# Kernel tuning notes

Hardware: AMD Instinct MI355X
Metric: run time of the kernel (lower is better)

## Reference

```python
import jax, jax.numpy as jnp
import numpy as np
from jax.scipy.linalg import expm

B, S, D_H, D_C = 8, 1024, 64, 3

def setup_inputs() -> dict:
    key = jax.random.key(0)
    k1, k2, k3 = jax.random.split(key, 3)
    x = jax.random.normal(k1, (B, S, D_H), dtype=jnp.float32)
    r_grid = jax.random.uniform(k2, (B, S, D_C), dtype=jnp.float32)
    L_param = jax.random.normal(k3, (D_C, D_H, D_H), dtype=jnp.float32)
    P_sp = jnp.eye(D_H, dtype=jnp.float32)  # allow_mixing=False -> identity buffer
    return {"x": x, "r_grid": r_grid, "L_param": L_param, "P_sp": P_sp}

def reference(x, r_grid, L_param, P_sp):
    # skew-symmetrize each generator: L_k <- 0.5*(L_k - L_k^T)
    L_skew = 0.5 * (L_param - jnp.swapaxes(L_param, -1, -2))      # [d_c, d_h, d_h]
    # A_r[b,s] = sum_k r_grid[b,s,k] * L_skew[k]
    A_r = jnp.einsum('bsk,kij->bsij', r_grid, L_skew)             # [B, S, d_h, d_h]
    # batched matrix exponential over leading dims
    R_r = expm(A_r)                                               # [B, S, d_h, d_h]
    R_eff = R_r @ P_sp                                            # [B, S, d_h, d_h]
    x_out = jnp.einsum('bsij,bsj->bsi', R_eff, x)                 # [B, S, d_h]
    return x_out
```

## Files before the change

### kernel.cpp

```cpp
#include <hip/hip_runtime.h>


typedef _Float16 half8 __attribute__((ext_vector_type(8)));
typedef __fp16 fp16x2 __attribute__((ext_vector_type(2)));
typedef float float4t __attribute__((ext_vector_type(4)));

union H2U { fp16x2 h; unsigned u; };

__device__ __forceinline__ unsigned pkrtz2(float a, float b) {
    H2U v; v.h = __builtin_amdgcn_cvt_pkrtz(a, b); return v.u;
}
__device__ __forceinline__ float h2lo(unsigned u) { H2U v; v.u = u; return (float)v.h[0]; }
__device__ __forceinline__ float h2hi(unsigned u) { H2U v; v.u = u; return (float)v.h[1]; }

__global__ void liepe_prep(const float* __restrict__ L, _Float16* __restrict__ wsA)
{
    int t = blockIdx.x * 256 + threadIdx.x;
    if (t >= 1536) return;
    int l   = t & 63;
    int f   = t >> 6;
    int kt  = f & 1;
    int m   = (f >> 1) & 3;
    int gen = f >> 3;
    int i   = 16 * m + (l & 15);
    int kk0 = 32 * kt + 8 * (l >> 4);
    const float* Lg = L + gen * 4096;
    half8 hi, lo;
    #pragma unroll
    for (int j = 0; j < 8; ++j) {
        int kk = kk0 + j;
        float d = Lg[i * 64 + kk] - Lg[kk * 64 + i];
        _Float16 h = (_Float16)d;
        hi[j] = h;
        lo[j] = (_Float16)(d - (float)h);
    }
    *(half8*)(wsA + f * 512 + l * 8) = hi;
    *(half8*)(wsA + 12288 + f * 512 + l * 8) = lo;
}


#define PSTR 36

#define STAGE_AND_LOAD_B()                                                       \
  {                                                                              \
    unsigned h0 = pkrtz2(b1[0], b1[1]);                                          \
    unsigned h1 = pkrtz2(b1[2], b1[3]);                                          \
    unsigned l0 = pkrtz2(b1[0] - h2lo(h0), b1[1] - h2hi(h0));                    \
    unsigned l1 = pkrtz2(b1[2] - h2lo(h1), b1[3] - h2hi(h1));                    \
    const int di = 8 * w + 2 * g;                                                \
    *(uint2*)&stage[buf][0][c][di] = make_uint2(h0, h1);                         \
    *(uint2*)&stage[buf][1][c][di] = make_uint2(l0, l1);                         \
    __syncthreads();                                                             \
    _Pragma("unroll")                                                            \
    for (int kt = 0; kt < 2; ++kt) {                                             \
      Bh[kt] = *(const half8*)&stage[buf][0][c][16 * kt + 4 * g];                \
      Bl[kt] = *(const half8*)&stage[buf][1][c][16 * kt + 4 * g];                \
    }                                                                            \
    buf ^= 1;                                                                    \
  }

#define GEMM_COMBINE(TOUT)                                                       \
  {                                                                              \
    _Pragma("unroll")                                                            \
    for (int gen = 0; gen < 3; ++gen) {                                          \
      float q = (gen == 0) ? q0 : ((gen == 1) ? q1 : q2);                        \
      float4t ac0 = {0.f, 0.f, 0.f, 0.f};                                        \
      float4t ac1 = {0.f, 0.f, 0.f, 0.f};                                        \
      ac0 = __builtin_amdgcn_mfma_f32_16x16x32_f16(Ah[gen*2+0], Bh[0], ac0, 0, 0, 0); \
      ac1 = __builtin_amdgcn_mfma_f32_16x16x32_f16(Ah[gen*2+1], Bh[1], ac1, 0, 0, 0); \
      ac0 = __builtin_amdgcn_mfma_f32_16x16x32_f16(Ah[gen*2+0], Bl[0], ac0, 0, 0, 0); \
      ac1 = __builtin_amdgcn_mfma_f32_16x16x32_f16(Ah[gen*2+1], Bl[1], ac1, 0, 0, 0); \
      ac0 = __builtin_amdgcn_mfma_f32_16x16x32_f16(Al[gen*2+0], Bh[0], ac0, 0, 0, 0); \
      ac1 = __builtin_amdgcn_mfma_f32_16x16x32_f16(Al[gen*2+1], Bh[1], ac1, 0, 0, 0); \
      _Pragma("unroll")                                                          \
      for (int r4 = 0; r4 < 4; ++r4) {                                           \
        float sum = ac0[r4] + ac1[r4];                                           \
        if (gen == 0) TOUT[r4] = q * sum;                                        \
        else          TOUT[r4] = fmaf(q, sum, TOUT[r4]);                         \
      }                                                                          \
    }                                                                            \
  }

__global__ __launch_bounds__(256) void liepe_mfma(
    const float* __restrict__ x,
    const float* __restrict__ r_grid,
    const _Float16* __restrict__ wsA,
    float* __restrict__ out,
    int n_tokens)
{
    __shared__ __align__(16) unsigned stage[2][2][16][PSTR];

    const int lane = threadIdx.x & 63;
    const int w    = threadIdx.x >> 6;
    const int c    = lane & 15;
    const int g    = lane >> 4;

    int tok = blockIdx.x * 16 + c;
    if (tok >= n_tokens) tok = n_tokens - 1;

    half8 Ah[6], Al[6];
    #pragma unroll
    for (int gen = 0; gen < 3; ++gen) {
        #pragma unroll
        for (int kt = 0; kt < 2; ++kt) {
            const int f = (gen * 4 + w) * 2 + kt;
            Ah[gen * 2 + kt] = *(const half8*)(wsA + f * 512 + lane * 8);
            Al[gen * 2 + kt] = *(const half8*)(wsA + 12288 + f * 512 + lane * 8);
        }
    }

    float xv[4];
    {
        float4 v = *(const float4*)(x + tok * 64 + 16 * w + 4 * g);
        xv[0] = v.x; xv[1] = v.y; xv[2] = v.z; xv[3] = v.w;
    }

    const float r0 = r_grid[tok * 3 + 0];
    const float r1 = r_grid[tok * 3 + 1];
    const float r2 = r_grid[tok * 3 + 2];
    const float sig2 = 0.5f * (r0 * r0 + r1 * r1 + r2 * r2);
    const float rho  = fmaf(17.3f, __builtin_sqrtf(sig2), 2.0f);
    const float inv_rho = 1.0f / rho;
    const int   M  = (int)rho + 14;
    const int   ms = M + 10;
    const float q0 = r0 * inv_rho, q1 = r1 * inv_rho, q2 = r2 * inv_rho;

    int maxM = M;
    #pragma unroll
    for (int off = 1; off < 64; off <<= 1)
        maxM = max(maxM, __shfl_xor(maxM, off));

    float jp = 0.f, jc = 0.f, N = 0.f;
    float b1[4] = {0.f, 0.f, 0.f, 0.f};
    float b2[4] = {0.f, 0.f, 0.f, 0.f};

    #pragma unroll 1
    for (int m = maxM + 10; m > maxM; --m) {
        bool sd = (m == ms);
        jc = sd ? 1e-12f : jc;
        jp = sd ? 0.f : jp;
        N  = sd ? (((m & 1) == 0) ? 2e-12f : 0.f) : N;
        float s = (jc > 1.0f) ? __builtin_amdgcn_rcpf(jc) : 1.0f;
        jc *= s; jp *= s; N *= s;
        float jm = fmaf((2.f * (float)m) * inv_rho, jc, -jp);
        jp = jc; jc = jm;
        int mm = m - 1;
        if ((mm & 1) == 0) N += (mm > 0) ? (jm + jm) : jm;
    }

    half8 Bh[2], Bl[2];
    int buf = 0;

    #pragma unroll 1
    for (int m = maxM; m >= 1; --m) {
        bool sd = (m == ms);
        jc = sd ? 1e-12f : jc;
        jp = sd ? 0.f : jp;
        N  = sd ? (((m & 1) == 0) ? 2e-12f : 0.f) : N;

        if (__any(jc > 2.0f)) {
            float s = (jc > 1.0f) ? __builtin_amdgcn_rcpf(jc) : 1.0f;
            jc *= s; jp *= s; N *= s;
            #pragma unroll
            for (int i = 0; i < 4; ++i) { b1[i] *= s; b2[i] *= s; }
        }

        STAGE_AND_LOAD_B();

        float t[4];
        GEMM_COMBINE(t);

        float cf = (m <= M) ? (jc + jc) : 0.f;
        #pragma unroll
        for (int i = 0; i < 4; ++i) {
            float bn = fmaf(cf, xv[i], t[i] + b2[i]);
            b2[i] = b1[i];
            b1[i] = bn;
        }

        float jm = fmaf((2.f * (float)m) * inv_rho, jc, -jp);
        jp = jc; jc = jm;
        int mm = m - 1;
        if ((mm & 1) == 0) N += (mm > 0) ? (jm + jm) : jm;
    }

    {
        STAGE_AND_LOAD_B();
        float t[4];
        GEMM_COMBINE(t);
        float4 v;
        float y0 = fmaf(jc, xv[0], t[0] + b2[0]);
        float y1 = fmaf(jc, xv[1], t[1] + b2[1]);
        float y2 = fmaf(jc, xv[2], t[2] + b2[2]);
        float y3 = fmaf(jc, xv[3], t[3] + b2[3]);
        v.x = (y0 - 0.5f * t[0]) / N;
        v.y = (y1 - 0.5f * t[1]) / N;
        v.z = (y2 - 0.5f * t[2]) / N;
        v.w = (y3 - 0.5f * t[3]) / N;
        *(float4*)(out + tok * 64 + 16 * w + 4 * g) = v;
    }
}

extern "C" void kernel_launch(void* const* d_in, const int* in_sizes, int n_in,
                              void* d_out, int out_size, void* d_ws, size_t ws_size,
                              hipStream_t stream) {
    const float* x = (const float*)d_in[0];
    const float* r = (const float*)d_in[1];
    const float* L = (const float*)d_in[2];
    float* out = (float*)d_out;
    _Float16* wsA = (_Float16*)d_ws;

    int n_tokens = in_sizes[0] / 64;

    liepe_prep<<<6, 256, 0, stream>>>(L, wsA);

    int nwg = (n_tokens + 15) / 16;
    liepe_mfma<<<nwg, 256, 0, stream>>>(x, r, wsA, out, n_tokens);
}
```

Baseline: 33.58 us.

## Unroll Clenshaw recurrence by two using precomputed generator products

The Bessel/Clenshaw recurrence now advances two steps per iteration. A new prep kernel precomputes the pairwise products of the skew generators (G_a G_b + G_b G_a), so each two-step update needs one barrier and a dependency chain of depth one instead of two serial matrix-vector stages. This halves the number of __syncthreads and sequential LDS round trips, but each iteration issues more MFMAs (12 matrix blocks versus 6), each thread holds 18 A-fragment pairs in registers, and occupancy is capped with waves_per_eu. The warp-uniform conditional rescale is replaced with an unconditional per-lane rescale.

```diff
diff --git a/kernel.cpp b/kernel.cpp
--- a/kernel.cpp
+++ b/kernel.cpp
@@ -13,82 +13,110 @@
 __device__ __forceinline__ float h2lo(unsigned u) { H2U v; v.u = u; return (float)v.h[0]; }
 __device__ __forceinline__ float h2hi(unsigned u) { H2U v; v.u = u; return (float)v.h[1]; }
 
-__global__ void liepe_prep(const float* __restrict__ L, _Float16* __restrict__ wsA)
+#define FRAG_LO 36864
+
+__global__ void liepe_prep_skew(const float* __restrict__ L, float* __restrict__ skew)
 {
     int t = blockIdx.x * 256 + threadIdx.x;
-    if (t >= 1536) return;
-    int l   = t & 63;
-    int f   = t >> 6;
-    int kt  = f & 1;
-    int m   = (f >> 1) & 3;
-    int gen = f >> 3;
-    int i   = 16 * m + (l & 15);
-    int kk0 = 32 * kt + 8 * (l >> 4);
-    const float* Lg = L + gen * 4096;
-    half8 hi, lo;
+    if (t >= 12288) return;
+    int k = t >> 12, rem = t & 4095, i = rem >> 6, j = rem & 63;
+    skew[t] = L[k * 4096 + i * 64 + j] - L[k * 4096 + j * 64 + i];
+}
+
+__global__ void liepe_prep_frags(const float* __restrict__ skew, _Float16* __restrict__ frag)
+{
+    const int p  = blockIdx.x >> 2;
+    const int m2 = blockIdx.x & 3;
+    __shared__ float Ga[4096], Gb[4096];
+    int a = 0, b = 0;
+    if (p >= 3) {
+        const int pa[6] = {0, 1, 2, 0, 0, 1};
+        const int pb[6] = {0, 1, 2, 1, 2, 2};
+        a = pa[p - 3]; b = pb[p - 3];
+        for (int idx = threadIdx.x; idx < 4096; idx += 256) {
+            Ga[idx] = skew[a * 4096 + idx];
+            Gb[idx] = skew[b * 4096 + idx];
+        }
+        __syncthreads();
+    }
     #pragma unroll
-    for (int j = 0; j < 8; ++j) {
-        int kk = kk0 + j;
-        float d = Lg[i * 64 + kk] - Lg[kk * 64 + i];
-        _Float16 h = (_Float16)d;
-        hi[j] = h;
-        lo[j] = (_Float16)(d - (float)h);
-    }
-    *(half8*)(wsA + f * 512 + l * 8) = hi;
-    *(half8*)(wsA + 12288 + f * 512 + l * 8) = lo;
+    for (int e4 = 0; e4 < 4; ++e4) {
+        int e = threadIdx.x * 4 + e4;
+        int kt = e >> 9, rem = e & 511, l = rem >> 3, j = rem & 7;
+        int i  = 16 * m2 + (l & 15);
+        int kk = 32 * kt + 8 * (l >> 4) + j;
+        float val;
+        if (p < 3) {
+            val = skew[p * 4096 + i * 64 + kk];
+        } else if (a == b) {
+            float acc = 0.f;
+            for (int t2 = 0; t2 < 64; ++t2)
+                acc += Ga[i * 64 + t2] * Ga[t2 * 64 + kk];
+            val = acc;
+        } else {
+            float acc = 0.f;
+            for (int t2 = 0; t2 < 64; ++t2)
+                acc += Ga[i * 64 + t2] * Gb[t2 * 64 + kk]
+                     + Gb[i * 64 + t2] * Ga[t2 * 64 + kk];
+            val = acc;
+        }
+        _Float16 h = (_Float16)val;
+        int f = p * 8 + m2 * 2 + kt;
+        frag[f * 512 + l * 8 + j] = h;
+        frag[FRAG_LO + f * 512 + l * 8 + j] = (_Float16)(val - (float)h);
+    }
 }
 
 
 #define PSTR 36
 
-#define STAGE_AND_LOAD_B()                                                       \
-  {                                                                              \
-    unsigned h0 = pkrtz2(b1[0], b1[1]);                                          \
-    unsigned h1 = pkrtz2(b1[2], b1[3]);                                          \
-    unsigned l0 = pkrtz2(b1[0] - h2lo(h0), b1[1] - h2hi(h0));                    \
-    unsigned l1 = pkrtz2(b1[2] - h2lo(h1), b1[3] - h2hi(h1));                    \
-    const int di = 8 * w + 2 * g;                                                \
-    *(uint2*)&stage[buf][0][c][di] = make_uint2(h0, h1);                         \
-    *(uint2*)&stage[buf][1][c][di] = make_uint2(l0, l1);                         \
-    __syncthreads();                                                             \
-    _Pragma("unroll")                                                            \
-    for (int kt = 0; kt < 2; ++kt) {                                             \
-      Bh[kt] = *(const half8*)&stage[buf][0][c][16 * kt + 4 * g];                \
-      Bl[kt] = *(const half8*)&stage[buf][1][c][16 * kt + 4 * g];                \
-    }                                                                            \
-    buf ^= 1;                                                                    \
-  }
-
-#define GEMM_COMBINE(TOUT)                                                       \
-  {                                                                              \
-    _Pragma("unroll")                                                            \
-    for (int gen = 0; gen < 3; ++gen) {                                          \
-      float q = (gen == 0) ? q0 : ((gen == 1) ? q1 : q2);                        \
-      float4t ac0 = {0.f, 0.f, 0.f, 0.f};                                        \
-      float4t ac1 = {0.f, 0.f, 0.f, 0.f};                                        \
-      ac0 = __builtin_amdgcn_mfma_f32_16x16x32_f16(Ah[gen*2+0], Bh[0], ac0, 0, 0, 0); \
-      ac1 = __builtin_amdgcn_mfma_f32_16x16x32_f16(Ah[gen*2+1], Bh[1], ac1, 0, 0, 0); \
-      ac0 = __builtin_amdgcn_mfma_f32_16x16x32_f16(Ah[gen*2+0], Bl[0], ac0, 0, 0, 0); \
-      ac1 = __builtin_amdgcn_mfma_f32_16x16x32_f16(Ah[gen*2+1], Bl[1], ac1, 0, 0, 0); \
-      ac0 = __builtin_amdgcn_mfma_f32_16x16x32_f16(Al[gen*2+0], Bh[0], ac0, 0, 0, 0); \
-      ac1 = __builtin_amdgcn_mfma_f32_16x16x32_f16(Al[gen*2+1], Bh[1], ac1, 0, 0, 0); \
-      _Pragma("unroll")                                                          \
-      for (int r4 = 0; r4 < 4; ++r4) {                                           \
-        float sum = ac0[r4] + ac1[r4];                                           \
-        if (gen == 0) TOUT[r4] = q * sum;                                        \
-        else          TOUT[r4] = fmaf(q, sum, TOUT[r4]);                         \
-      }                                                                          \
-    }                                                                            \
-  }
-
-__global__ __launch_bounds__(256) void liepe_mfma(
+#define STAGE_VEC(VEC, BV)                                                    \
+  { unsigned h0 = pkrtz2(BV[0], BV[1]);                                       \
+    unsigned h1 = pkrtz2(BV[2], BV[3]);                                       \
+    unsigned l0 = pkrtz2(BV[0] - h2lo(h0), BV[1] - h2hi(h0));                 \
+    unsigned l1 = pkrtz2(BV[2] - h2lo(h1), BV[3] - h2hi(h1));                 \
+    const int di = 8 * w + 2 * g;                                             \
+    *(uint2*)&stage[buf][VEC][0][c][di] = make_uint2(h0, h1);                 \
+    *(uint2*)&stage[buf][VEC][1][c][di] = make_uint2(l0, l1); }
+
+#define LOAD_VEC(VEC, BH, BL)                                                 \
+  { _Pragma("unroll")                                                         \
+    for (int kt = 0; kt < 2; ++kt) {                                          \
+      BH[kt] = *(const half8*)&stage[buf][VEC][0][c][16 * kt + 4 * g];        \
+      BL[kt] = *(const half8*)&stage[buf][VEC][1][c][16 * kt + 4 * g];        \
+    } }
+
+#define MAT_ACC(P, BH, BL, Q, TOUT, FIRST)                                    \
+  { float4t ac0 = {0.f, 0.f, 0.f, 0.f};                                       \
+    float4t ac1 = {0.f, 0.f, 0.f, 0.f};                                       \
+    ac0 = __builtin_amdgcn_mfma_f32_16x16x32_f16(Ah[(P)*2+0], BH[0], ac0, 0, 0, 0); \
+    ac1 = __builtin_amdgcn_mfma_f32_16x16x32_f16(Ah[(P)*2+1], BH[1], ac1, 0, 0, 0); \
+    ac0 = __builtin_amdgcn_mfma_f32_16x16x32_f16(Ah[(P)*2+0], BL[0], ac0, 0, 0, 0); \
+    ac1 = __builtin_amdgcn_mfma_f32_16x16x32_f16(Ah[(P)*2+1], BL[1], ac1, 0, 0, 0); \
+    ac0 = __builtin_amdgcn_mfma_f32_16x16x32_f16(Al[(P)*2+0], BH[0], ac0, 0, 0, 0); \
+    ac1 = __builtin_amdgcn_mfma_f32_16x16x32_f16(Al[(P)*2+1], BH[1], ac1, 0, 0, 0); \
+    _Pragma("unroll")                                                         \
+    for (int r4 = 0; r4 < 4; ++r4) {                                          \
+      float sum = ac0[r4] + ac1[r4];                                          \
+      if (FIRST) TOUT[r4] = (Q) * sum;                                        \
+      else       TOUT[r4] = fmaf((Q), sum, TOUT[r4]);                         \
+    } }
+
+#define GEMM_Z(BH, BL, TOUT)                                                  \
+  MAT_ACC(0, BH, BL, q0, TOUT, true)                                          \
+  MAT_ACC(1, BH, BL, q1, TOUT, false)                                         \
+  MAT_ACC(2, BH, BL, q2, TOUT, false)
+
+__global__ __launch_bounds__(256)
+__attribute__((amdgpu_waves_per_eu(1, 2)))
+void liepe_mfma(
     const float* __restrict__ x,
     const float* __restrict__ r_grid,
-    const _Float16* __restrict__ wsA,
+    const _Float16* __restrict__ frag,
     float* __restrict__ out,
     int n_tokens)
 {
-    __shared__ __align__(16) unsigned stage[2][2][16][PSTR];
+    __shared__ __align__(16) unsigned stage[2][2][2][16][PSTR];
 
     const int lane = threadIdx.x & 63;
     const int w    = threadIdx.x >> 6;
@@ -98,14 +126,14 @@
     int tok = blockIdx.x * 16 + c;
     if (tok >= n_tokens) tok = n_tokens - 1;
 
-    half8 Ah[6], Al[6];
+    half8 Ah[18], Al[18];
     #pragma unroll
-    for (int gen = 0; gen < 3; ++gen) {
+    for (int p = 0; p < 9; ++p) {
         #pragma unroll
         for (int kt = 0; kt < 2; ++kt) {
-            const int f = (gen * 4 + w) * 2 + kt;
-            Ah[gen * 2 + kt] = *(const half8*)(wsA + f * 512 + lane * 8);
-            Al[gen * 2 + kt] = *(const half8*)(wsA + 12288 + f * 512 + lane * 8);
+            const int f = p * 8 + w * 2 + kt;
+            Ah[p * 2 + kt] = *(const half8*)(frag + f * 512 + lane * 8);
+            Al[p * 2 + kt] = *(const half8*)(frag + FRAG_LO + f * 512 + lane * 8);
         }
     }
 
@@ -124,6 +152,8 @@
     const int   M  = (int)rho + 14;
     const int   ms = M + 10;
     const float q0 = r0 * inv_rho, q1 = r1 * inv_rho, q2 = r2 * inv_rho;
+    const float p00 = q0 * q0, p11 = q1 * q1, p22 = q2 * q2;
+    const float p01 = q0 * q1, p02 = q0 * q2, p12 = q1 * q2;
 
     int maxM = M;
     #pragma unroll
@@ -131,8 +161,6 @@
         maxM = max(maxM, __shfl_xor(maxM, off));
 
     float jp = 0.f, jc = 0.f, N = 0.f;
-    float b1[4] = {0.f, 0.f, 0.f, 0.f};
-    float b2[4] = {0.f, 0.f, 0.f, 0.f};
 
     #pragma unroll 1
     for (int m = maxM + 10; m > maxM; --m) {
@@ -148,55 +176,121 @@
         if ((mm & 1) == 0) N += (mm > 0) ? (jm + jm) : jm;
     }
 
-    half8 Bh[2], Bl[2];
     int buf = 0;
 
+    float zx[4];
+    {
+        STAGE_VEC(0, xv);
+        __syncthreads();
+        half8 Xh[2], Xl[2];
+        LOAD_VEC(0, Xh, Xl);
+        GEMM_Z(Xh, Xl, zx);
+        buf = 1;
+    }
+
+    float B1v[4] = {0.f, 0.f, 0.f, 0.f};
+    float B2v[4] = {0.f, 0.f, 0.f, 0.f};
+
+    int m = maxM;
     #pragma unroll 1
-    for (int m = maxM; m >= 1; --m) {
+    while (m >= 2) {
         bool sd = (m == ms);
         jc = sd ? 1e-12f : jc;
         jp = sd ? 0.f : jp;
         N  = sd ? (((m & 1) == 0) ? 2e-12f : 0.f) : N;
 
-        if (__any(jc > 2.0f)) {
-            float s = (jc > 1.0f) ? __builtin_amdgcn_rcpf(jc) : 1.0f;
-            jc *= s; jp *= s; N *= s;
-            #pragma unroll
-            for (int i = 0; i < 4; ++i) { b1[i] *= s; b2[i] *= s; }
-        }
-
-        STAGE_AND_LOAD_B();
-
-        float t[4];
-        GEMM_COMBINE(t);
-
-        float cf = (m <= M) ? (jc + jc) : 0.f;
-        #pragma unroll
-        for (int i = 0; i < 4; ++i) {
-            float bn = fmaf(cf, xv[i], t[i] + b2[i]);
-            b2[i] = b1[i];
-            b1[i] = bn;
-        }
-
+        float s = (jc > 1.0f) ? __builtin_amdgcn_rcpf(jc) : 1.0f;
+        jc *= s; jp *= s; N *= s;
+        #pragma unroll
+        for (int i = 0; i < 4; ++i) { B1v[i] *= s; B2v[i] *= s; }
+
+        STAGE_VEC(0, B1v);
+        STAGE_VEC(1, B2v);
+        __syncthreads();
+        half8 B1h[2], B1l[2], B2h[2], B2l[2];
+        LOAD_VEC(0, B1h, B1l);
+        LOAD_VEC(1, B2h, B2l);
+        buf ^= 1;
+
+        float u[4];
+        GEMM_Z(B1h, B1l, u);
+        float vw[4];
+        MAT_ACC(3, B1h, B1l, p00, vw, true)
+        MAT_ACC(4, B1h, B1l, p11, vw, false)
+        MAT_ACC(5, B1h, B1l, p22, vw, false)
+        MAT_ACC(6, B1h, B1l, p01, vw, false)
+        MAT_ACC(7, B1h, B1l, p02, vw, false)
+        MAT_ACC(8, B1h, B1l, p12, vw, false)
+        MAT_ACC(0, B2h, B2l, q0, vw, false)
+        MAT_ACC(1, B2h, B2l, q1, vw, false)
+        MAT_ACC(2, B2h, B2l, q2, vw, false)
+
+        float cfm = (m <= M) ? (jc + jc) : 0.f;
         float jm = fmaf((2.f * (float)m) * inv_rho, jc, -jp);
         jp = jc; jc = jm;
-        int mm = m - 1;
-        if ((mm & 1) == 0) N += (mm > 0) ? (jm + jm) : jm;
+        { int mm = m - 1; if ((mm & 1) == 0) N += (mm > 0) ? (jm + jm) : jm; }
+
+        bool sd1 = ((m - 1) == ms);
+        jc = sd1 ? 1e-12f : jc;
+        jp = sd1 ? 0.f : jp;
+        N  = sd1 ? ((((m - 1) & 1) == 0) ? 2e-12f : 0.f) : N;
+        float cfm1 = ((m - 1) <= M) ? (jc + jc) : 0.f;
+
+        float nbm[4], nbm1[4];
+        #pragma unroll
+        for (int i = 0; i < 4; ++i) {
+            nbm[i]  = fmaf(cfm,  xv[i], u[i] + B2v[i]);
+            nbm1[i] = fmaf(cfm1, xv[i], fmaf(cfm, zx[i], vw[i] + B1v[i]));
+        }
+
+        jm = fmaf((2.f * (float)(m - 1)) * inv_rho, jc, -jp);
+        jp = jc; jc = jm;
+        { int mm = m - 2; if ((mm & 1) == 0) N += (mm > 0) ? (jm + jm) : jm; }
+
+        #pragma unroll
+        for (int i = 0; i < 4; ++i) { B2v[i] = nbm[i]; B1v[i] = nbm1[i]; }
+        m -= 2;
+    }
+
+    if (m == 1) {
+        float s = (jc > 1.0f) ? __builtin_amdgcn_rcpf(jc) : 1.0f;
+        jc *= s; jp *= s; N *= s;
+        #pragma unroll
+        for (int i = 0; i < 4; ++i) { B1v[i] *= s; B2v[i] *= s; }
+        STAGE_VEC(0, B1v);
+        __syncthreads();
+        half8 B1h[2], B1l[2];
+        LOAD_VEC(0, B1h, B1l);
+        buf ^= 1;
+        float u[4];
+        GEMM_Z(B1h, B1l, u);
+        float cf = jc + jc;
+        float nb[4];
+        #pragma unroll
+        for (int i = 0; i < 4; ++i) nb[i] = fmaf(cf, xv[i], u[i] + B2v[i]);
+        float jm = fmaf(2.f * inv_rho, jc, -jp);
+        jp = jc; jc = jm;
+        N += jm;
+        #pragma unroll
+        for (int i = 0; i < 4; ++i) { B2v[i] = B1v[i]; B1v[i] = nb[i]; }
     }
 
     {
-        STAGE_AND_LOAD_B();
+        float s = (jc > 1.0f) ? __builtin_amdgcn_rcpf(jc) : 1.0f;
+        jc *= s; jp *= s; N *= s;
+        #pragma unroll
+        for (int i = 0; i < 4; ++i) { B1v[i] *= s; B2v[i] *= s; }
+        STAGE_VEC(0, B1v);
+        __syncthreads();
+        half8 B1h[2], B1l[2];
+        LOAD_VEC(0, B1h, B1l);
         float t[4];
-        GEMM_COMBINE(t);
+        GEMM_Z(B1h, B1l, t);
         float4 v;
-        float y0 = fmaf(jc, xv[0], t[0] + b2[0]);
-        float y1 = fmaf(jc, xv[1], t[1] + b2[1]);
-        float y2 = fmaf(jc, xv[2], t[2] + b2[2]);
-        float y3 = fmaf(jc, xv[3], t[3] + b2[3]);
-        v.x = (y0 - 0.5f * t[0]) / N;
-        v.y = (y1 - 0.5f * t[1]) / N;
-        v.z = (y2 - 0.5f * t[2]) / N;
-        v.w = (y3 - 0.5f * t[3]) / N;
+        v.x = (fmaf(jc, xv[0], t[0] + B2v[0]) - 0.5f * t[0]) / N;
+        v.y = (fmaf(jc, xv[1], t[1] + B2v[1]) - 0.5f * t[1]) / N;
+        v.z = (fmaf(jc, xv[2], t[2] + B2v[2]) - 0.5f * t[2]) / N;
+        v.w = (fmaf(jc, xv[3], t[3] + B2v[3]) - 0.5f * t[3]) / N;
         *(float4*)(out + tok * 64 + 16 * w + 4 * g) = v;
     }
 }
@@ -208,12 +302,15 @@
     const float* r = (const float*)d_in[1];
     const float* L = (const float*)d_in[2];
     float* out = (float*)d_out;
-    _Float16* wsA = (_Float16*)d_ws;
+
+    float*     skew = (float*)d_ws;
+    _Float16*  frag = (_Float16*)d_ws + 24576;
 
     int n_tokens = in_sizes[0] / 64;
 
-    liepe_prep<<<6, 256, 0, stream>>>(L, wsA);
+    liepe_prep_skew<<<48, 256, 0, stream>>>(L, skew);
+    liepe_prep_frags<<<36, 256, 0, stream>>>(skew, frag);
 
     int nwg = (n_tokens + 15) / 16;
-    liepe_mfma<<<nwg, 256, 0, stream>>>(x, r, wsA, out, n_tokens);
-}
+    liepe_mfma<<<nwg, 256, 0, stream>>>(x, r, frag, out, n_tokens);
+}
```

Result: slower. 67.58 us (+101.3%).
